# Optimization experiments

Measured on AMD Instinct MI355X. Metric: run time of the kernel, lower is better.

## Reference

```python
import jax, jax.numpy as jnp
import numpy as np

HEAD_NUM = 16
QKV_DIM = 32
EMB = 512
SQRT_EMB = 22.627416997969522  # sqrt(512)
LOGIT_CLIP = 10.0
BATCH, POMO, PROBLEM = 32, 256, 1024


def setup_inputs() -> dict:
    key = jax.random.key(0)
    ks = jax.random.split(key, 8)
    s = 0.02
    return {
        "encoded_nodes": jax.random.normal(ks[0], (BATCH, PROBLEM, EMB), jnp.float32),
        "encoded_q1": jax.random.normal(ks[1], (BATCH, POMO, EMB), jnp.float32),
        "encoded_last_node": jax.random.normal(ks[2], (BATCH, POMO, EMB), jnp.float32),
        "ninf_mask": jnp.zeros((BATCH, POMO, PROBLEM), jnp.float32),
        # weights stored [in, out] so y = x @ W (equiv. to torch Linear with W.T)
        "Wq_first": jax.random.normal(ks[3], (EMB, HEAD_NUM * QKV_DIM), jnp.float32) * s,
        "Wq_last": jax.random.normal(ks[4], (EMB, HEAD_NUM * QKV_DIM), jnp.float32) * s,
        "Wk": jax.random.normal(ks[5], (EMB, HEAD_NUM * QKV_DIM), jnp.float32) * s,
        "Wv": jax.random.normal(ks[6], (EMB, HEAD_NUM * QKV_DIM), jnp.float32) * s,
        "W_combine": jax.random.normal(ks[7], (HEAD_NUM * QKV_DIM, EMB), jnp.float32) * s,
        "b_combine": jnp.zeros((EMB,), jnp.float32),
    }


def _heads(x):
    # [b, n, h*d] -> [b, h, n, d]
    b, n, _ = x.shape
    return x.reshape(b, n, HEAD_NUM, QKV_DIM).transpose(0, 2, 1, 3)


def reference(encoded_nodes, encoded_q1, encoded_last_node, ninf_mask,
              Wq_first, Wq_last, Wk, Wv, W_combine, b_combine):
    # set_kv
    k = _heads(encoded_nodes @ Wk)                     # [b,h,problem,d]
    v = _heads(encoded_nodes @ Wv)                     # [b,h,problem,d]
    single_head_key = encoded_nodes.transpose(0, 2, 1) # [b,emb,problem]
    # set_q1
    q_first = _heads(encoded_q1 @ Wq_first)            # [b,h,pomo,d]
    # forward
    q_last = _heads(encoded_last_node @ Wq_last)       # [b,h,pomo,d]
    q = q_first + q_last

    scale = 1.0 / jnp.sqrt(jnp.asarray(QKV_DIM, q.dtype))
    score = jnp.einsum("bhnd,bhmd->bhnm", q, k) * scale  # [b,h,pomo,problem]
    score = score + ninf_mask[:, None, :, :]
    weights = jax.nn.softmax(score, axis=-1)
    out = jnp.einsum("bhnm,bhmd->bhnd", weights, v)      # [b,h,pomo,d]
    out_concat = out.transpose(0, 2, 1, 3).reshape(q.shape[0], q.shape[2], HEAD_NUM * QKV_DIM)
    mh_out = out_concat @ W_combine + b_combine          # [b,pomo,emb]

    score2 = jnp.einsum("bne,bem->bnm", mh_out, single_head_key) / SQRT_EMB
    score2 = LOGIT_CLIP * jnp.tanh(score2) + ninf_mask
    probs = jax.nn.softmax(score2, axis=2)               # [b,pomo,problem]
    return probs
```

## Files before the change

kernel.cpp:

```cpp
#include <hip/hip_runtime.h>
#include <math.h>

typedef unsigned short u16;
typedef __attribute__((ext_vector_type(8))) short bf16x8;
typedef __attribute__((ext_vector_type(4))) float f32x4;
typedef __attribute__((ext_vector_type(4))) int i32x4;
typedef __attribute__((ext_vector_type(4))) short s16x4;
typedef __attribute__((ext_vector_type(4))) unsigned short u16x4;

#define MFMA16(a,b,c) __builtin_amdgcn_mfma_f32_16x16x32_bf16((a),(b),(c),0,0,0)

__device__ __forceinline__ u16 f2bf(float x){
  unsigned int u = __float_as_uint(x);
  u += 0x7fffu + ((u >> 16) & 1u);
  return (u16)(u >> 16);
}
__device__ __forceinline__ float bf2f(u16 x){
  return __uint_as_float(((unsigned)x) << 16);
}
__device__ __forceinline__ void gload16(const void* g, void* l){
  __builtin_amdgcn_global_load_lds((const __attribute__((address_space(1))) void*)g,
                                   (__attribute__((address_space(3))) void*)l, 16, 0, 0);
}

__global__ __launch_bounds__(256) void prep(
    const float* __restrict__ nodes, const float* __restrict__ q1, const float* __restrict__ lastn,
    const float* __restrict__ mask,
    const float* __restrict__ Wqf, const float* __restrict__ Wql, const float* __restrict__ Wk,
    const float* __restrict__ Wv, const float* __restrict__ Wc,
    u16* __restrict__ nodesb, u16* __restrict__ qlb,
    u16* __restrict__ WtKV, u16* __restrict__ WtQ2, u16* __restrict__ WtC,
    u16* __restrict__ maskP)
{
  const int tid = blockIdx.x * 256 + threadIdx.x;
  const int NT = 1048576;
  for (int i = tid; i < 4194304; i += NT) {
    float4 v = ((const float4*)nodes)[i];
    u16x4 o; o[0]=f2bf(v.x); o[1]=f2bf(v.y); o[2]=f2bf(v.z); o[3]=f2bf(v.w);
    *(u16x4*)&nodesb[i*4] = o;
  }
  {
    const int m = tid >> 7, k4 = (tid & 127)*4;
    float4 v = ((const float4*)q1)[tid];
    u16x4 o; o[0]=f2bf(v.x); o[1]=f2bf(v.y); o[2]=f2bf(v.z); o[3]=f2bf(v.w);
    *(u16x4*)&qlb[m*1024 + k4] = o;
    v = ((const float4*)lastn)[tid];
    o[0]=f2bf(v.x); o[1]=f2bf(v.y); o[2]=f2bf(v.z); o[3]=f2bf(v.w);
    *(u16x4*)&qlb[m*1024 + 512 + k4] = o;
  }
  if (tid < 262144) {
    int n = tid >> 9, k = tid & 511;
    WtQ2[n*1024 + k]       = f2bf(Wqf[k*512 + n]);
    WtQ2[n*1024 + 512 + k] = f2bf(Wql[k*512 + n]);
    WtC[tid]  = f2bf(Wc[k*512 + n]);
  }
  if (tid < 524288) {
    int n = tid >> 9, k = tid & 511;
    WtKV[tid] = f2bf(n < 512 ? Wk[k*512 + n] : Wv[k*512 + (n-512)]);
  }
  if (tid < 524288) {
    int brt = tid >> 10, c = tid & 1023;
    const float* mp = mask + (brt*16)*1024 + c;
    u16 vals[16];
    #pragma unroll
    for (int p=0;p<16;p++) vals[p] = f2bf(mp[p*1024]);
    *(i32x4*)&maskP[tid*16]     = *(i32x4*)&vals[0];
    *(i32x4*)&maskP[tid*16 + 8] = *(i32x4*)&vals[8];
  }
}

__global__ __launch_bounds__(512, 2) void kvq(
    const u16* __restrict__ Akv, const u16* __restrict__ Bkv,
    const u16* __restrict__ Aq,  const u16* __restrict__ Bq,
    u16* __restrict__ Kout, u16* __restrict__ Vout, u16* __restrict__ Qout)
{
  __shared__ u16 smem[24576];
  const int t = threadIdx.x, w = t >> 6, l = t & 63, q = l >> 4, ln = l & 15;
  const int wr = w >> 2, wc = w & 3;
  const int wm = wr * 64, wn = wc * 64;

  const bool isq = blockIdx.x < 128;
  int mb, nb, ksteps, kstr;
  const u16 *Ab, *Bb;
  if (isq) {
    const int bid = blockIdx.x;
    mb = bid >> 1; nb = bid & 1;
    ksteps = 32; kstr = 1024; Ab = Aq; Bb = Bq;
  } else {
    const int bid = blockIdx.x - 128;
    mb = (bid >> 5)*8 + (bid & 7);
    nb = (bid >> 3) & 3;
    ksteps = 16; kstr = 512; Ab = Akv; Bb = Bkv;
  }
  const int m0 = mb*128, n0 = nb*256;

  f32x4 acc[4][4];
  #pragma unroll
  for (int i=0;i<4;i++)
    #pragma unroll
    for (int j=0;j<4;j++)
      #pragma unroll
      for (int r=0;r<4;r++) acc[i][j][r] = 0.f;

  const u16* Aaddr = Ab + (m0 + (t & 127))*kstr + (t >> 7)*8;
  const u16* Baddr = Bb + (n0 + (t & 255))*kstr + (t >> 8)*8;

  #define STAGE(kc_, b_) { \
    u16* s = smem + (b_)*12288; \
    gload16(Aaddr + (kc_)*32,      &s[t*8]); \
    gload16(Baddr + (kc_)*32,      &s[4096 + t*8]); \
    gload16(Baddr + 16 + (kc_)*32, &s[4096 + (t+512)*8]); }

  STAGE(0, 0);
  for (int kc = 0; kc < ksteps; kc++) {
    __syncthreads();
    if (kc + 1 < ksteps) STAGE(kc+1, (kc+1)&1);
    const u16* sa = smem + (kc&1)*12288;
    const u16* sb = sa + 4096;
    bf16x8 af[4], bfr[4];
    #pragma unroll
    for (int i=0;i<4;i++) af[i]  = *(bf16x8*)&sa[(q*128 + wm + i*16 + ln)*8];
    #pragma unroll
    for (int j=0;j<4;j++) bfr[j] = *(bf16x8*)&sb[(q*256 + wn + j*16 + ln)*8];
    #pragma unroll
    for (int i=0;i<4;i++)
      #pragma unroll
      for (int j=0;j<4;j++)
        acc[i][j] = MFMA16(af[i], bfr[j], acc[i][j]);
  }
  #undef STAGE

  const float scale = isq ? 0.17677669529663687f : 1.0f;
  const int bb_ = mb >> 3, mloc = (mb & 7)*128;
  const int bbq = mb >> 1, pm0 = (mb & 1)*128;
  for (int h = 0; h < 4; ++h) {
    __syncthreads();
    if (wc == h) {
      #pragma unroll
      for (int i=0;i<4;i++)
        #pragma unroll
        for (int j=0;j<4;j++) {
          s16x4 o;
          #pragma unroll
          for (int r=0;r<4;r++) o[r] = (short)f2bf(acc[i][j][r]*scale);
          *(s16x4*)&smem[(j*16 + ln)*140 + wm + i*16 + q*4] = o;
        }
    }
    __syncthreads();
    #pragma unroll
    for (int hc=0; hc<2; ++hc) {
      if (isq) {
        const int head = nb*8 + h*2 + hc;
        const int m_ = t >> 2, d0 = (t & 3)*8;
        u16 v[8];
        #pragma unroll
        for (int dd=0;dd<8;dd++) v[dd] = smem[(hc*32 + d0 + dd)*140 + m_];
        *(i32x4*)&Qout[((bbq*16 + head)*256 + pm0 + m_)*32 + d0] = *(i32x4*)&v[0];
      } else if (nb < 2) {
        const int head = nb*8 + h*2 + hc;
        const int m_ = t >> 2, d0 = (t & 3)*8;
        u16 v[8];
        #pragma unroll
        for (int dd=0;dd<8;dd++) v[dd] = smem[(hc*32 + d0 + dd)*140 + m_];
        *(i32x4*)&Kout[((bb_*16 + head)*1024 + mloc + m_)*32 + d0] = *(i32x4*)&v[0];
      } else {
        const int vh = (nb-2)*8 + h*2 + hc;
        const int d = t >> 4, mo = (t & 15)*8;
        *(i32x4*)&Vout[((bb_*16 + vh)*32 + d)*1024 + mloc + mo]
            = *(i32x4*)&smem[(hc*32 + d)*140 + mo];
      }
    }
  }
}

__global__ __launch_bounds__(256) void attn(const u16* __restrict__ Qg, const u16* __restrict__ Kg,
                                            const u16* __restrict__ Vtg, const u16* __restrict__ maskP,
                                            u16* __restrict__ Og)
{
  const int bid = blockIdx.x;
  const int bh = (bid >> 5)*8 + (bid & 7);
  const int pt = (bid >> 3) & 3;
  const int h = bh & 15, bb = bh >> 4;
  const int t = threadIdx.x, w = t >> 6, l = t & 63, q = l >> 4, ln = l & 15;
  __shared__ u16 Qs[2048];
  __shared__ u16 Ks[4096];
  __shared__ u16 Vs[4096];
  __shared__ u16 Ps[4*640];
  u16* Pw = &Ps[w*640];
  const int qbase = ((bb*16 + h)*256 + pt*64)*32;
  gload16(&Qg[qbase + (t & 63)*32 + (t >> 6)*8], &Qs[t*8]);
  const int kbase = (bb*16 + h)*1024*32;
  const int vbase = (bb*16 + h)*32*1024;
  float rs[4] = {0.f,0.f,0.f,0.f};
  f32x4 oacc[2];
  #pragma unroll
  for (int dt=0;dt<2;dt++)
    #pragma unroll
    for (int r=0;r<4;r++) oacc[dt][r] = 0.f;
  __syncthreads();
  const bf16x8 aq = *(bf16x8*)&Qs[(q*64 + w*16 + ln)*8];
  const u16* mrow = maskP + (bb*16 + pt*4 + w)*16384 + q*4;
  for (int mc = 0; mc < 8; mc++) {
    __syncthreads();
    gload16(&Kg[kbase + (mc*128 + (t & 127))*32 + (t >> 7)*8],       &Ks[t*8]);
    gload16(&Kg[kbase + (mc*128 + (t & 127))*32 + ((t >> 7)+2)*8],   &Ks[(t+256)*8]);
    gload16(&Vtg[vbase + (t & 31)*1024 + mc*128 + (t >> 5)*8],       &Vs[t*8]);
    gload16(&Vtg[vbase + (t & 31)*1024 + mc*128 + ((t >> 5)+8)*8],   &Vs[(t+256)*8]);
    u16x4 mq[8];
    #pragma unroll
    for (int j2=0;j2<8;j2++)
      mq[j2] = *(const u16x4*)&mrow[(mc*128 + j2*16 + ln)*16];
    __syncthreads();
    #pragma unroll
    for (int ch=0; ch<4; ch++) {
      bf16x8 bk0 = *(bf16x8*)&Ks[(q*128 + (ch*2+0)*16 + ln)*8];
      bf16x8 bk1 = *(bf16x8*)&Ks[(q*128 + (ch*2+1)*16 + ln)*8];
      f32x4 zz = {0.f,0.f,0.f,0.f};
      f32x4 s0 = MFMA16(aq, bk0, zz);
      f32x4 s1 = MFMA16(aq, bk1, zz);
      #pragma unroll
      for (int r=0;r<4;r++) {
        float e0 = __expf(s0[r] + bf2f(mq[ch*2+0][r]));
        float e1 = __expf(s1[r] + bf2f(mq[ch*2+1][r]));
        rs[r] += e0 + e1;
        Pw[(q*4+r)*40 + ln]      = f2bf(e0);
        Pw[(q*4+r)*40 + 16 + ln] = f2bf(e1);
      }
      bf16x8 ap  = *(bf16x8*)&Pw[ln*40 + q*8];
      bf16x8 bv0 = *(bf16x8*)&Vs[((ch*4+q)*32 + ln)*8];
      bf16x8 bv1 = *(bf16x8*)&Vs[((ch*4+q)*32 + 16 + ln)*8];
      oacc[0] = MFMA16(ap, bv0, oacc[0]);
      oacc[1] = MFMA16(ap, bv1, oacc[1]);
    }
  }
  #pragma unroll
  for (int r=0;r<4;r++) {
    float v = rs[r];
    v += __shfl_xor(v,1); v += __shfl_xor(v,2); v += __shfl_xor(v,4); v += __shfl_xor(v,8);
    rs[r] = __builtin_amdgcn_rcpf(v);
  }
  const int orow = bb*256 + pt*64 + w*16 + q*4;
  #pragma unroll
  for (int dt=0;dt<2;dt++)
    #pragma unroll
    for (int r=0;r<4;r++)
      Og[(orow + r)*512 + h*32 + dt*16 + ln] = f2bf(oacc[dt][r]*rs[r]);
}

__global__ __launch_bounds__(1024) void cmbfin(const u16* __restrict__ oc, const u16* __restrict__ WtC,
                                               const float* __restrict__ bias,
                                               const u16* __restrict__ nodesb, const u16* __restrict__ maskP,
                                               float* __restrict__ out)
{
  const int bid = blockIdx.x;
  const int bb = bid & 31, rg = bid >> 5;
  const int t = threadIdx.x, w = t >> 6, l = t & 63, q = l >> 4, ln = l & 15;
  __shared__ u16 As[16384];
  __shared__ u16 Ms[16384];
  __shared__ float rsL[16][32];
  const int abase = (bb*256 + rg*32)*512;
  #pragma unroll
  for (int c=0;c<2;c++) {
    int chunk = t + 1024*c;
    gload16(&oc[abase + (chunk & 31)*512 + (chunk >> 5)*8], &As[chunk*8]);
  }
  __syncthreads();
  f32x4 acc1[2][2];
  #pragma unroll
  for (int i=0;i<2;i++)
    #pragma unroll
    for (int ct=0;ct<2;ct++)
      #pragma unroll
      for (int r=0;r<4;r++) acc1[i][ct][r] = 0.f;
  for (int kc=0;kc<16;kc++) {
    bf16x8 af[2];
    #pragma unroll
    for (int i=0;i<2;i++) af[i] = *(bf16x8*)&As[((kc*4 + q)*32 + i*16 + ln)*8];
    #pragma unroll
    for (int ct=0;ct<2;ct++) {
      int col = w*32 + ct*16 + ln;
      bf16x8 bfr = *(const bf16x8*)&WtC[col*512 + kc*32 + q*8];
      #pragma unroll
      for (int i=0;i<2;i++) acc1[i][ct] = MFMA16(af[i], bfr, acc1[i][ct]);
    }
  }
  #pragma unroll
  for (int ct=0;ct<2;ct++) {
    int gn = w*32 + ct*16 + ln;
    float bv = bias[gn];
    #pragma unroll
    for (int i=0;i<2;i++)
      #pragma unroll
      for (int r=0;r<4;r++)
        Ms[(gn >> 3)*256 + (i*16 + q*4 + r)*8 + (gn & 7)] = f2bf(acc1[i][ct][r] + bv);
  }
  __syncthreads();
  float rloc[2][4] = {{0.f,0.f,0.f,0.f},{0.f,0.f,0.f,0.f}};
  const int nbase = bb*524288;
  f32x4 acc[2][4];
  #pragma unroll
  for (int i=0;i<2;i++)
    #pragma unroll
    for (int ct=0;ct<4;ct++)
      #pragma unroll
      for (int r=0;r<4;r++) acc[i][ct][r] = 0.f;
  for (int kc=0;kc<16;kc++) {
    bf16x8 af[2];
    #pragma unroll
    for (int i=0;i<2;i++) af[i] = *(bf16x8*)&Ms[((kc*4 + q)*32 + i*16 + ln)*8];
    #pragma unroll
    for (int ct=0;ct<4;ct++) {
      int col = w*64 + ct*16 + ln;
      bf16x8 bfr = *(const bf16x8*)&nodesb[nbase + col*512 + kc*32 + q*8];
      #pragma unroll
      for (int i=0;i<2;i++) acc[i][ct] = MFMA16(af[i], bfr, acc[i][ct]);
    }
  }
  const float c2 = 0.08838834764831843f;
  const int prow_base = bb*256 + rg*32;
  #pragma unroll
  for (int i=0;i<2;i++) {
    #pragma unroll
    for (int ct=0;ct<4;ct++) {
      int col0 = w*64 + ct*16 + ln;
      u16x4 mv = *(const u16x4*)&maskP[((bb*16 + rg*2 + i)*1024 + col0)*16 + q*4];
      #pragma unroll
      for (int r=0;r<4;r++) {
        float x = acc[i][ct][r] * c2;
        x = fminf(fmaxf(x, -30.f), 30.f);
        float e2 = __expf(x);
        float lg = 10.f*(e2 - 1.f)*__builtin_amdgcn_rcpf(e2 + 1.f) + bf2f(mv[r]);
        float e = __expf(lg);
        rloc[i][r] += e;
        acc[i][ct][r] = e;
      }
    }
  }
  #pragma unroll
  for (int i=0;i<2;i++)
    #pragma unroll
    for (int r=0;r<4;r++) {
      float v = rloc[i][r];
      v += __shfl_xor(v,1); v += __shfl_xor(v,2); v += __shfl_xor(v,4); v += __shfl_xor(v,8);
      rloc[i][r] = v;
    }
  if (ln == 0) {
    #pragma unroll
    for (int i=0;i<2;i++)
      #pragma unroll
      for (int r=0;r<4;r++) rsL[w][i*16 + q*4 + r] = rloc[i][r];
  }
  __syncthreads();
  float inv[2][4];
  #pragma unroll
  for (int i=0;i<2;i++)
    #pragma unroll
    for (int r=0;r<4;r++) {
      float tot = 0.f;
      #pragma unroll
      for (int ww=0;ww<16;ww++) tot += rsL[ww][i*16 + q*4 + r];
      inv[i][r] = __builtin_amdgcn_rcpf(tot);
    }
  #pragma unroll
  for (int i=0;i<2;i++)
    #pragma unroll
    for (int ct=0;ct<4;ct++) {
      int col0 = w*64 + ct*16 + ln;
      #pragma unroll
      for (int r=0;r<4;r++)
        out[(prow_base + i*16 + q*4 + r)*1024 + col0] = acc[i][ct][r]*inv[i][r];
    }
}

extern "C" void kernel_launch(void* const* d_in, const int* in_sizes, int n_in,
                              void* d_out, int out_size, void* d_ws, size_t ws_size,
                              hipStream_t stream)
{
  (void)in_sizes; (void)n_in; (void)out_size; (void)ws_size;
  const float* nodes = (const float*)d_in[0];
  const float* q1    = (const float*)d_in[1];
  const float* lastn = (const float*)d_in[2];
  const float* mask  = (const float*)d_in[3];
  const float* Wqf   = (const float*)d_in[4];
  const float* Wql   = (const float*)d_in[5];
  const float* Wk    = (const float*)d_in[6];
  const float* Wv    = (const float*)d_in[7];
  const float* Wc    = (const float*)d_in[8];
  const float* bias  = (const float*)d_in[9];
  float* out = (float*)d_out;

  char* p = (char*)d_ws;
  u16* nodesb = (u16*)p; p += 33554432;
  u16* qlb    = (u16*)p; p += 16777216;
  u16* WtKV   = (u16*)p; p += 1048576;
  u16* WtQ2   = (u16*)p; p += 1048576;
  u16* WtC    = (u16*)p; p += 524288;
  u16* Kt     = (u16*)p; p += 33554432;
  u16* Vt     = (u16*)p; p += 33554432;
  u16* Qh     = (u16*)p; p += 8388608;
  u16* maskP  = (u16*)p; p += 16777216;
  u16* oc  = qlb;

  prep<<<4096, 256, 0, stream>>>(nodes, q1, lastn, mask, Wqf, Wql, Wk, Wv, Wc,
                                 nodesb, qlb, WtKV, WtQ2, WtC, maskP);
  kvq<<<1152, 512, 0, stream>>>(nodesb, WtKV, qlb, WtQ2, Kt, Vt, Qh);
  attn<<<2048, 256, 0, stream>>>(Qh, Kt, Vt, maskP, oc);
  cmbfin<<<256, 1024, 0, stream>>>(oc, WtC, bias, nodesb, maskP, out);
}
```

Measured before the change: 373.2 us.

## Process all 256 pomo rows per attention block to reuse K/V tiles

Each attention block now handles a whole (batch, head) pair: it loads all 256 query rows and processes four 16-row groups per wave against each K/V tile. This cuts global K/V traffic fourfold, since previously four blocks reloaded the same K/V. Mask loads for the next row group are double-buffered (software prefetch) across the groups. The cost is a quarter as many blocks (512), more accumulator registers per thread and lower occupancy and parallelism.

```diff
diff --git a/kernel.cpp b/kernel.cpp
--- a/kernel.cpp
+++ b/kernel.cpp
@@ -178,73 +178,98 @@
                                             u16* __restrict__ Og)
 {
   const int bid = blockIdx.x;
-  const int bh = (bid >> 5)*8 + (bid & 7);
-  const int pt = (bid >> 3) & 3;
+  const int bh = (bid & 7)*64 + (bid >> 3);
   const int h = bh & 15, bb = bh >> 4;
   const int t = threadIdx.x, w = t >> 6, l = t & 63, q = l >> 4, ln = l & 15;
-  __shared__ u16 Qs[2048];
+  __shared__ u16 Qs[8192];
   __shared__ u16 Ks[4096];
   __shared__ u16 Vs[4096];
-  __shared__ u16 Ps[4*640];
+  __shared__ u16 Ps[2560];
   u16* Pw = &Ps[w*640];
-  const int qbase = ((bb*16 + h)*256 + pt*64)*32;
-  gload16(&Qg[qbase + (t & 63)*32 + (t >> 6)*8], &Qs[t*8]);
+  const int qbase = (bb*16 + h)*256*32;
+  #pragma unroll
+  for (int c=0;c<4;c++)
+    gload16(&Qg[qbase + t*32 + c*8], &Qs[(c*256 + t)*8]);
   const int kbase = (bb*16 + h)*1024*32;
   const int vbase = (bb*16 + h)*32*1024;
-  float rs[4] = {0.f,0.f,0.f,0.f};
-  f32x4 oacc[2];
-  #pragma unroll
-  for (int dt=0;dt<2;dt++)
-    #pragma unroll
-    for (int r=0;r<4;r++) oacc[dt][r] = 0.f;
+  float rs[4][4];
+  f32x4 oacc[4][2];
+  #pragma unroll
+  for (int rg=0;rg<4;rg++) {
+    #pragma unroll
+    for (int r=0;r<4;r++) rs[rg][r] = 0.f;
+    #pragma unroll
+    for (int dt=0;dt<2;dt++)
+      #pragma unroll
+      for (int r=0;r<4;r++) oacc[rg][dt][r] = 0.f;
+  }
   __syncthreads();
-  const bf16x8 aq = *(bf16x8*)&Qs[(q*64 + w*16 + ln)*8];
-  const u16* mrow = maskP + (bb*16 + pt*4 + w)*16384 + q*4;
+  bf16x8 aq[4];
+  #pragma unroll
+  for (int rg=0;rg<4;rg++) aq[rg] = *(bf16x8*)&Qs[(q*256 + w*64 + rg*16 + ln)*8];
+  const u16* mbase = maskP + (bb*16 + w*4)*16384 + q*4;
+  u16x4 mqA[8], mqB[8];
+
+  #define RG_BODY(rg, MQC, MQN) { \
+    if ((rg) < 3) { \
+      _Pragma("unroll") \
+      for (int j2=0;j2<8;j2++) \
+        MQN[j2] = *(const u16x4*)&mbase[((rg)+1)*16384 + (mc*128 + j2*16 + ln)*16]; \
+    } \
+    _Pragma("unroll") \
+    for (int ch=0; ch<4; ch++) { \
+      bf16x8 bk0 = *(bf16x8*)&Ks[(q*128 + (ch*2+0)*16 + ln)*8]; \
+      bf16x8 bk1 = *(bf16x8*)&Ks[(q*128 + (ch*2+1)*16 + ln)*8]; \
+      f32x4 zz = {0.f,0.f,0.f,0.f}; \
+      f32x4 s0 = MFMA16(aq[rg], bk0, zz); \
+      f32x4 s1 = MFMA16(aq[rg], bk1, zz); \
+      _Pragma("unroll") \
+      for (int r=0;r<4;r++) { \
+        float e0 = __expf(s0[r] + bf2f(MQC[ch*2+0][r])); \
+        float e1 = __expf(s1[r] + bf2f(MQC[ch*2+1][r])); \
+        rs[rg][r] += e0 + e1; \
+        Pw[(q*4+r)*40 + ln]      = f2bf(e0); \
+        Pw[(q*4+r)*40 + 16 + ln] = f2bf(e1); \
+      } \
+      bf16x8 ap  = *(bf16x8*)&Pw[ln*40 + q*8]; \
+      bf16x8 bv0 = *(bf16x8*)&Vs[((ch*4+q)*32 + ln)*8]; \
+      bf16x8 bv1 = *(bf16x8*)&Vs[((ch*4+q)*32 + 16 + ln)*8]; \
+      oacc[rg][0] = MFMA16(ap, bv0, oacc[rg][0]); \
+      oacc[rg][1] = MFMA16(ap, bv1, oacc[rg][1]); \
+    } }
+
   for (int mc = 0; mc < 8; mc++) {
     __syncthreads();
     gload16(&Kg[kbase + (mc*128 + (t & 127))*32 + (t >> 7)*8],       &Ks[t*8]);
     gload16(&Kg[kbase + (mc*128 + (t & 127))*32 + ((t >> 7)+2)*8],   &Ks[(t+256)*8]);
     gload16(&Vtg[vbase + (t & 31)*1024 + mc*128 + (t >> 5)*8],       &Vs[t*8]);
     gload16(&Vtg[vbase + (t & 31)*1024 + mc*128 + ((t >> 5)+8)*8],   &Vs[(t+256)*8]);
-    u16x4 mq[8];
     #pragma unroll
     for (int j2=0;j2<8;j2++)
-      mq[j2] = *(const u16x4*)&mrow[(mc*128 + j2*16 + ln)*16];
+      mqA[j2] = *(const u16x4*)&mbase[(mc*128 + j2*16 + ln)*16];
     __syncthreads();
-    #pragma unroll
-    for (int ch=0; ch<4; ch++) {
-      bf16x8 bk0 = *(bf16x8*)&Ks[(q*128 + (ch*2+0)*16 + ln)*8];
-      bf16x8 bk1 = *(bf16x8*)&Ks[(q*128 + (ch*2+1)*16 + ln)*8];
-      f32x4 zz = {0.f,0.f,0.f,0.f};
-      f32x4 s0 = MFMA16(aq, bk0, zz);
-      f32x4 s1 = MFMA16(aq, bk1, zz);
-      #pragma unroll
-      for (int r=0;r<4;r++) {
-        float e0 = __expf(s0[r] + bf2f(mq[ch*2+0][r]));
-        float e1 = __expf(s1[r] + bf2f(mq[ch*2+1][r]));
-        rs[r] += e0 + e1;
-        Pw[(q*4+r)*40 + ln]      = f2bf(e0);
-        Pw[(q*4+r)*40 + 16 + ln] = f2bf(e1);
-      }
-      bf16x8 ap  = *(bf16x8*)&Pw[ln*40 + q*8];
-      bf16x8 bv0 = *(bf16x8*)&Vs[((ch*4+q)*32 + ln)*8];
-      bf16x8 bv1 = *(bf16x8*)&Vs[((ch*4+q)*32 + 16 + ln)*8];
-      oacc[0] = MFMA16(ap, bv0, oacc[0]);
-      oacc[1] = MFMA16(ap, bv1, oacc[1]);
-    }
-  }
-  #pragma unroll
-  for (int r=0;r<4;r++) {
-    float v = rs[r];
-    v += __shfl_xor(v,1); v += __shfl_xor(v,2); v += __shfl_xor(v,4); v += __shfl_xor(v,8);
-    rs[r] = __builtin_amdgcn_rcpf(v);
-  }
-  const int orow = bb*256 + pt*64 + w*16 + q*4;
-  #pragma unroll
-  for (int dt=0;dt<2;dt++)
-    #pragma unroll
-    for (int r=0;r<4;r++)
-      Og[(orow + r)*512 + h*32 + dt*16 + ln] = f2bf(oacc[dt][r]*rs[r]);
+    RG_BODY(0, mqA, mqB)
+    RG_BODY(1, mqB, mqA)
+    RG_BODY(2, mqA, mqB)
+    RG_BODY(3, mqB, mqA)
+  }
+  #undef RG_BODY
+
+  #pragma unroll
+  for (int rg=0;rg<4;rg++) {
+    #pragma unroll
+    for (int r=0;r<4;r++) {
+      float v = rs[rg][r];
+      v += __shfl_xor(v,1); v += __shfl_xor(v,2); v += __shfl_xor(v,4); v += __shfl_xor(v,8);
+      rs[rg][r] = __builtin_amdgcn_rcpf(v);
+    }
+    const int orow = bb*256 + w*64 + rg*16 + q*4;
+    #pragma unroll
+    for (int dt=0;dt<2;dt++)
+      #pragma unroll
+      for (int r=0;r<4;r++)
+        Og[(orow + r)*512 + h*32 + dt*16 + ln] = f2bf(oacc[rg][dt][r]*rs[rg][r]);
+  }
 }
 
 __global__ __launch_bounds__(1024) void cmbfin(const u16* __restrict__ oc, const u16* __restrict__ WtC,
@@ -404,6 +429,6 @@
   prep<<<4096, 256, 0, stream>>>(nodes, q1, lastn, mask, Wqf, Wql, Wk, Wv, Wc,
                                  nodesb, qlb, WtKV, WtQ2, WtC, maskP);
   kvq<<<1152, 512, 0, stream>>>(nodesb, WtKV, qlb, WtQ2, Kt, Vt, Qh);
-  attn<<<2048, 256, 0, stream>>>(Qh, Kt, Vt, maskP, oc);
+  attn<<<512, 256, 0, stream>>>(Qh, Kt, Vt, maskP, oc);
   cmbfin<<<256, 1024, 0, stream>>>(oc, WtC, bias, nodesb, maskP, out);
 }
```

Result: no change. 374.4 us (+0.3%).
